# Optimization experiments

Measured on AMD Instinct MI355X. Metric: run time of the kernel, lower is better.

The kernel has to match this reference:

```python
import jax, jax.numpy as jnp
from jax import lax
import numpy as np

NEG_INF = -10000.0
MAX_W = 15          # max_span_width for every marker
M = 5               # num_markers
H = 1024            # encoder hidden size (deberta-v3-large)
B, N = 16, 2048


def _gelu(x):
    return jax.nn.gelu(x, approximate=False)  # torch nn.GELU default (erf)


def _consistency(scores, mask, gamma, width_logits):
    # scores: [B, N] token scores for one marker; mask: [B, N] int
    n = scores.shape[1]
    masked = jnp.where(mask == 0, NEG_INF, scores)
    ww = jax.nn.softmax(width_logits)  # [MAX_W]
    boosts = [masked]
    for w in range(2, min(MAX_W, n) + 1):
        # sliding-window min of width w -> span_mins [B, n-w+1]
        mins = lax.reduce_window(masked, float('inf'), lax.min,
                                 (1, w), (1, 1), 'VALID')
        weighted = mins * ww[w - 2]
        # expand each span-min back to every token it covers via sliding max
        p = jnp.pad(weighted, ((0, 0), (w - 1, w - 1)), constant_values=NEG_INF)
        expanded = lax.reduce_window(p, float('-inf'), lax.max,
                                     (1, w), (1, 1), 'VALID')  # [B, n]
        boosts.append(expanded)
    boost = jnp.max(jnp.stack(boosts, axis=0), axis=0)
    return scores + gamma * boost


def setup_inputs() -> dict:
    key = jax.random.key(0)
    ks = jax.random.split(key, 12)
    s = 0.02
    inp = {
        'h': jax.random.normal(ks[0], (B, N, H), jnp.float32),
        'attention_mask': jnp.ones((B, N), jnp.int32),
        # per-marker token scorers, stacked on leading marker axis
        'W1': jax.random.normal(ks[1], (M, H, 512), jnp.float32) * s,
        'b1': jnp.zeros((M, 512), jnp.float32),
        'W2': jax.random.normal(ks[2], (M, 512, 256), jnp.float32) * s,
        'b2': jnp.zeros((M, 256), jnp.float32),
        'W3': jax.random.normal(ks[3], (M, 256), jnp.float32) * s,
        'b3': jnp.zeros((M,), jnp.float32),
        # span-consistency params
        'gamma': jnp.ones((M,), jnp.float32),
        'width_logits': jax.random.normal(ks[4], (M, MAX_W), jnp.float32) * 0.1,
        # cross-marker attention params
        'corr': jnp.eye(M, dtype=jnp.float32) * 0.5,
        'cw1': jax.random.normal(ks[5], (M, 64), jnp.float32) * 0.1,
        'cb1': jnp.zeros((64,), jnp.float32),
        'cw2': jax.random.normal(ks[6], (64, M), jnp.float32) * 0.1,
        'cb2': jnp.zeros((M,), jnp.float32),
        'gate': jnp.array(0.3, jnp.float32),
    }
    return inp


def reference(h, attention_mask, W1, b1, W2, b2, W3, b3,
              gamma, width_logits, corr, cw1, cb1, cw2, cb2, gate):
    # token scorers (dropout is identity in eval): [M, B, N]
    t1 = _gelu(jnp.einsum('bnh,mhd->mbnd', h, W1) + b1[:, None, None, :])
    t2 = _gelu(jnp.einsum('mbnd,mde->mbne', t1, W2) + b2[:, None, None, :])
    scores = jnp.einsum('mbne,me->mbn', t2, W3) + b3[:, None, None]
    # per-marker span-consistency boost
    boosted = jax.vmap(_consistency, in_axes=(0, None, 0, 0))(
        scores, attention_mask, gamma, width_logits)      # [M, B, N]
    logits = jnp.transpose(boosted, (1, 2, 0))            # [B, N, M]
    # cross-marker attention
    probs = jax.nn.sigmoid(logits)
    correlated = probs @ corr
    refined = _gelu(correlated @ cw1 + cb1) @ cw2 + cb2
    return logits + jax.nn.sigmoid(gate) * refined
```

## Files before the change

kernel.cpp:

```cpp
#include <hip/hip_runtime.h>
#include <math.h>


typedef __bf16 bf16x8 __attribute__((ext_vector_type(8)));
typedef float f32x4 __attribute__((ext_vector_type(4)));

#define NEG_INF_VAL (-10000.0f)

__device__ __forceinline__ unsigned short f2bf(float f) {
  union { float f; unsigned u; } v; v.f = f;
  unsigned r = v.u + 0x7fffu + ((v.u >> 16) & 1u);
  return (unsigned short)(r >> 16);
}
__device__ __forceinline__ float bf2f(unsigned short b) {
  union { unsigned u; float f; } v; v.u = ((unsigned)b) << 16;
  return v.f;
}
__device__ __forceinline__ float gelu_erf(float x) {
  return 0.5f * x * (1.0f + erff(x * 0.7071067811865476f));
}
__device__ __forceinline__ float gelu_fast(float x) {
  float u = 0.7978845608f * x * (1.0f + 0.044715f * x * x);
  float e = __expf(-2.0f * fabsf(u));
  float t = (1.0f - e) / (1.0f + e);
  t = copysignf(t, u);
  return 0.5f * x * (1.0f + t);
}

__global__ __launch_bounds__(256) void k_f32_to_bf16x4(
    const float* __restrict__ in, unsigned short* __restrict__ out, int n4) {
  int i = blockIdx.x * 256 + threadIdx.x;
  if (i >= n4) return;
  float4 v = reinterpret_cast<const float4*>(in)[i];
  ushort4 o;
  o.x = f2bf(v.x); o.y = f2bf(v.y); o.z = f2bf(v.z); o.w = f2bf(v.w);
  reinterpret_cast<ushort4*>(out)[i] = o;
}

__global__ __launch_bounds__(256) void k_transpose_tiled(
    const float* __restrict__ W, unsigned short* __restrict__ Wt,
    int K, int C) {
  __shared__ float tile[32][33];
  const int m = blockIdx.z;
  const int c0 = blockIdx.x * 32, k0 = blockIdx.y * 32;
  const int tx = threadIdx.x & 31, ty = threadIdx.x >> 5;
  const float* Wm = W + (size_t)m * K * C;
#pragma unroll
  for (int r = ty; r < 32; r += 8)
    tile[r][tx] = Wm[(size_t)(k0 + r) * C + c0 + tx];
  __syncthreads();
  unsigned short* Wtm = Wt + (size_t)m * C * K;
#pragma unroll
  for (int r = ty; r < 32; r += 8)
    Wtm[(size_t)(c0 + r) * K + k0 + tx] = f2bf(tile[tx][r]);
}

__device__ __forceinline__ void stage_tile(
    const unsigned short* __restrict__ A, size_t lda,
    const unsigned short* __restrict__ B, size_t ldb,
    int rowA0, int rowB0, int k0,
    unsigned short* As, unsigned short* Bs, int w, int l) {
  const int r = l & 15;
  const int c8 = (l >> 4) * 8;
#pragma unroll
  for (int h = 0; h < 2; ++h) {
    const unsigned short* ga = A + (size_t)(rowA0 + h * 128 + w * 16 + r) * lda + k0 + c8;
    unsigned short* da = As + (h * 8 + w) * 1024 + l * 8;
    __builtin_amdgcn_global_load_lds((const __attribute__((address_space(1))) void*)ga,
                                     (__attribute__((address_space(3))) void*)da, 16, 0, 0);
    __builtin_amdgcn_global_load_lds((const __attribute__((address_space(1))) void*)(ga + 32),
                                     (__attribute__((address_space(3))) void*)(da + 512), 16, 0, 0);
    const unsigned short* gb = B + (size_t)(rowB0 + h * 128 + w * 16 + r) * ldb + k0 + c8;
    unsigned short* db = Bs + (h * 8 + w) * 1024 + l * 8;
    __builtin_amdgcn_global_load_lds((const __attribute__((address_space(1))) void*)gb,
                                     (__attribute__((address_space(3))) void*)db, 16, 0, 0);
    __builtin_amdgcn_global_load_lds((const __attribute__((address_space(1))) void*)(gb + 32),
                                     (__attribute__((address_space(3))) void*)(db + 512), 16, 0, 0);
  }
}

template <bool FUSE_SCORES>
__global__ __launch_bounds__(512) void k_gemm256(
    const unsigned short* __restrict__ A, int lda, int aOffPerM,
    const unsigned short* __restrict__ Bt, int K,
    const float* __restrict__ bias,
    unsigned short* __restrict__ C, int ldc,
    const float* __restrict__ W3, const float* __restrict__ b3,
    float* __restrict__ scoresOut,
    int tilesPerM, int colsPerM, int nColTiles) {
  __shared__ __align__(16) unsigned short As[2][16384];
  __shared__ __align__(16) unsigned short Bs[2][16384];
  __shared__ float sc[256];
  const int t512 = threadIdx.x;
  const int w = t512 >> 6, l = t512 & 63;
  const int wr = w >> 2, wc = w & 3;

  const int nwg = gridDim.x;
  const int cpx = nwg >> 3;
  const int bid = blockIdx.x;
  const int swz = (bid & 7) * cpx + (bid >> 3);
  const int ct = swz % nColTiles, rt = swz / nColTiles;
  const int m = ct / tilesPerM, cb = ct - m * tilesPerM;
  const int gcol0 = m * colsPerM + cb * 256;
  const int row0 = rt * 256;
  const unsigned short* Am = A + (size_t)m * aOffPerM;

  if (FUSE_SCORES && t512 < 256) sc[t512] = 0.f;

  f32x4 acc[8][4] = {};
  const int NT = K >> 6;

  stage_tile(Am, lda, Bt, K, row0, gcol0, 0, As[0], Bs[0], w, l);
  stage_tile(Am, lda, Bt, K, row0, gcol0, 64, As[1], Bs[1], w, l);
  asm volatile("s_waitcnt vmcnt(8)" ::: "memory");
  __builtin_amdgcn_sched_barrier(0);
  __builtin_amdgcn_s_barrier();
  __builtin_amdgcn_sched_barrier(0);

  for (int t = 0; t < NT; ++t) {
    const int p = t & 1;
    bf16x8 af[8][2], bf[4][2];
#pragma unroll
    for (int i = 0; i < 8; ++i)
#pragma unroll
      for (int ks = 0; ks < 2; ++ks)
        af[i][ks] = *reinterpret_cast<const bf16x8*>(&As[p][(wr * 8 + i) * 1024 + ks * 512 + l * 8]);
#pragma unroll
    for (int j = 0; j < 4; ++j)
#pragma unroll
      for (int ks = 0; ks < 2; ++ks)
        bf[j][ks] = *reinterpret_cast<const bf16x8*>(&Bs[p][(wc * 4 + j) * 1024 + ks * 512 + l * 8]);
    asm volatile("s_waitcnt lgkmcnt(0)" ::: "memory");
    __builtin_amdgcn_sched_barrier(0);
    __builtin_amdgcn_s_barrier();
    __builtin_amdgcn_sched_barrier(0);
    if (t + 2 < NT)
      stage_tile(Am, lda, Bt, K, row0, gcol0, (t + 2) * 64, As[p], Bs[p], w, l);
    __builtin_amdgcn_sched_barrier(0);
    __builtin_amdgcn_s_setprio(1);
#pragma unroll
    for (int ks = 0; ks < 2; ++ks)
#pragma unroll
      for (int i = 0; i < 8; ++i)
#pragma unroll
        for (int j = 0; j < 4; ++j)
          acc[i][j] = __builtin_amdgcn_mfma_f32_16x16x32_bf16(af[i][ks], bf[j][ks], acc[i][j], 0, 0, 0);
    __builtin_amdgcn_s_setprio(0);
    __builtin_amdgcn_sched_barrier(0);
    if (t + 1 < NT) {
      if (t + 2 < NT) { asm volatile("s_waitcnt vmcnt(8)" ::: "memory"); }
      else            { asm volatile("s_waitcnt vmcnt(0)" ::: "memory"); }
      __builtin_amdgcn_sched_barrier(0);
      __builtin_amdgcn_s_barrier();
      __builtin_amdgcn_sched_barrier(0);
    }
  }

  if (!FUSE_SCORES) {
    const int orow = (l >> 4) * 4, ocol = l & 15;
#pragma unroll
    for (int i = 0; i < 8; ++i)
#pragma unroll
      for (int j = 0; j < 4; ++j) {
        const int gc = gcol0 + wc * 64 + j * 16 + ocol;
        const float bv = bias[gc];
        const int gr0 = row0 + wr * 128 + i * 16 + orow;
#pragma unroll
        for (int r = 0; r < 4; ++r) {
          float v = gelu_fast(acc[i][j][r] + bv);
          C[(size_t)(gr0 + r) * ldc + gc] = f2bf(v);
        }
      }
  } else {
    const int ocol = l & 15;
#pragma unroll
    for (int i = 0; i < 8; ++i) {
      float rs[4] = {0.f, 0.f, 0.f, 0.f};
#pragma unroll
      for (int j = 0; j < 4; ++j) {
        const int cl = wc * 64 + j * 16 + ocol;
        const float bv = bias[m * 256 + cl];
        const float w3v = W3[m * 256 + cl];
#pragma unroll
        for (int r = 0; r < 4; ++r)
          rs[r] += gelu_fast(acc[i][j][r] + bv) * w3v;
      }
#pragma unroll
      for (int s = 1; s < 16; s <<= 1)
#pragma unroll
        for (int r = 0; r < 4; ++r)
          rs[r] += __shfl_xor(rs[r], s);
      if (ocol == 0) {
        const int lr0 = wr * 128 + i * 16 + (l >> 4) * 4;
#pragma unroll
        for (int r = 0; r < 4; ++r)
          atomicAdd(&sc[lr0 + r], rs[r]);
      }
    }
    __syncthreads();
    if (t512 < 256)
      scoresOut[(size_t)m * 32768 + row0 + t512] = sc[t512] + b3[m];
  }
}

__global__ __launch_bounds__(256) void k_span(
    const float* __restrict__ scores,
    const int* __restrict__ mask,
    const float* __restrict__ gamma,
    const float* __restrict__ wlog,
    float* __restrict__ logits) {
  const int b = blockIdx.x, m = blockIdx.y;
  const int tid = threadIdx.x;
  __shared__ float masked[2048], mins[2048], boost[2048];
  __shared__ float ww[14];
  if (tid == 0) {
    float mx = -1e30f;
    for (int i = 0; i < 15; i++) mx = fmaxf(mx, wlog[m * 15 + i]);
    float e[15], sum = 0.f;
    for (int i = 0; i < 15; i++) { e[i] = expf(wlog[m * 15 + i] - mx); sum += e[i]; }
    for (int i = 0; i < 14; i++) ww[i] = e[i] / sum;
  }
  const float* srow = scores + ((size_t)m * 16 + b) * 2048;
  const int* mrow = mask + (size_t)b * 2048;
  for (int i = tid; i < 2048; i += 256) {
    float s = srow[i];
    float mk = (mrow[i] == 0) ? NEG_INF_VAL : s;
    masked[i] = mk; mins[i] = mk; boost[i] = mk;
  }
  __syncthreads();
  for (int w2 = 2; w2 <= 15; w2++) {
    for (int s = tid; s <= 2048 - w2; s += 256)
      mins[s] = fminf(mins[s], masked[s + w2 - 1]);
    __syncthreads();
    float c = ww[w2 - 2];
    for (int i = tid; i < 2048; i += 256) {
      int lo = i - w2 + 1; if (lo < 0) lo = 0;
      int hi = i; if (hi > 2048 - w2) hi = 2048 - w2;
      float mx = -1e30f;
      for (int s = lo; s <= hi; s++) mx = fmaxf(mx, mins[s]);
      boost[i] = fmaxf(boost[i], mx * c);
    }
    __syncthreads();
  }
  float g = gamma[m];
  for (int i = tid; i < 2048; i += 256)
    logits[((size_t)b * 2048 + i) * 5 + m] = srow[i] + g * boost[i];
}

__global__ __launch_bounds__(256) void k_cross(
    const float* __restrict__ logits, const float* __restrict__ corr,
    const float* __restrict__ cw1, const float* __restrict__ cb1,
    const float* __restrict__ cw2, const float* __restrict__ cb2,
    const float* __restrict__ gate, float* __restrict__ out) {
  __shared__ float s_corr[25], s_cw1[320], s_cb1[64], s_cw2[320], s_cb2[5];
  int tid = threadIdx.x;
  if (tid < 25) s_corr[tid] = corr[tid];
  if (tid < 64) s_cb1[tid] = cb1[tid];
  if (tid < 5)  s_cb2[tid] = cb2[tid];
  for (int i = tid; i < 320; i += 256) { s_cw1[i] = cw1[i]; s_cw2[i] = cw2[i]; }
  __syncthreads();
  int t = blockIdx.x * 256 + tid;
  float lg[5], pr[5];
#pragma unroll
  for (int m = 0; m < 5; m++) {
    lg[m] = logits[(size_t)t * 5 + m];
    pr[m] = 1.f / (1.f + expf(-lg[m]));
  }
  float co[5];
#pragma unroll
  for (int j = 0; j < 5; j++) {
    float s = 0.f;
#pragma unroll
    for (int mm = 0; mm < 5; mm++) s += pr[mm] * s_corr[mm * 5 + j];
    co[j] = s;
  }
  float ref[5];
#pragma unroll
  for (int m = 0; m < 5; m++) ref[m] = s_cb2[m];
  for (int k = 0; k < 64; k++) {
    float h = s_cb1[k];
#pragma unroll
    for (int j = 0; j < 5; j++) h += co[j] * s_cw1[j * 64 + k];
    h = gelu_erf(h);
#pragma unroll
    for (int m = 0; m < 5; m++) ref[m] += h * s_cw2[k * 5 + m];
  }
  float sg = 1.f / (1.f + expf(-gate[0]));
#pragma unroll
  for (int m = 0; m < 5; m++) out[(size_t)t * 5 + m] = lg[m] + sg * ref[m];
}

extern "C" void kernel_launch(void* const* d_in, const int* in_sizes, int n_in,
                              void* d_out, int out_size, void* d_ws, size_t ws_size,
                              hipStream_t stream) {
  const float* h     = (const float*)d_in[0];
  const int*   mask  = (const int*)d_in[1];
  const float* W1    = (const float*)d_in[2];
  const float* b1    = (const float*)d_in[3];
  const float* W2    = (const float*)d_in[4];
  const float* b2    = (const float*)d_in[5];
  const float* W3    = (const float*)d_in[6];
  const float* b3    = (const float*)d_in[7];
  const float* gamma = (const float*)d_in[8];
  const float* wlog  = (const float*)d_in[9];
  const float* corr  = (const float*)d_in[10];
  const float* cw1   = (const float*)d_in[11];
  const float* cb1   = (const float*)d_in[12];
  const float* cw2   = (const float*)d_in[13];
  const float* cb2   = (const float*)d_in[14];
  const float* gate  = (const float*)d_in[15];
  float* out = (float*)d_out;

  char* ws = (char*)d_ws;
  unsigned short* hb  = (unsigned short*)(ws);
  unsigned short* W1t = (unsigned short*)(ws + 67108864);
  unsigned short* W2t = (unsigned short*)(ws + 72351744);
  unsigned short* t1  = (unsigned short*)(ws + 73662464);
  float* scores       = (float*)(ws + 241434624);
  float* logits       = (float*)(ws + 242089984);

  k_f32_to_bf16x4<<<33554432 / 4 / 256, 256, 0, stream>>>(h, hb, 33554432 / 4);
  k_transpose_tiled<<<dim3(16, 32, 5), 256, 0, stream>>>(W1, W1t, 1024, 512);
  k_transpose_tiled<<<dim3(8, 16, 5), 256, 0, stream>>>(W2, W2t, 512, 256);

  k_gemm256<false><<<1280, 512, 0, stream>>>(
      hb, 1024, 0, W1t, 1024, b1, t1, 2560,
      nullptr, nullptr, nullptr, 10, 2560, 10);
  k_gemm256<true><<<640, 512, 0, stream>>>(
      t1, 2560, 512, W2t, 512, b2, nullptr, 0,
      W3, b3, scores, 1, 256, 5);

  k_span<<<dim3(16, 5), 256, 0, stream>>>(scores, mask, gamma, wlog, logits);
  k_cross<<<32768 / 256, 256, 0, stream>>>(logits, corr, cw1, cb1, cw2, cb2, gate, out);
}
```

Baseline: 679.6 us.

## Restructure GEMM mainloop into four sub-phases with interleaved half-tile prefetch

The GEMM main loop is rewritten so each 64-wide K tile is split into four phases (two K halves by two row halves). Each phase loads fewer fragments from LDS, issues part of the next tile's global-to-LDS copies, then runs 16 MFMAs. The trip count becomes a template parameter and the loop is unrolled by two with explicit tail tiles, and pointer increments replace per-stage address recomputation. The goal is to cut register pressure and spread memory traffic across the MFMA stream, at the cost of many more barriers per tile and fragile hand-counted vmcnt values.

```diff
diff --git a/kernel.cpp b/kernel.cpp
--- a/kernel.cpp
+++ b/kernel.cpp
@@ -55,31 +55,112 @@
     Wtm[(size_t)(c0 + r) * K + k0 + tx] = f2bf(tile[tx][r]);
 }
 
-__device__ __forceinline__ void stage_tile(
-    const unsigned short* __restrict__ A, size_t lda,
-    const unsigned short* __restrict__ B, size_t ldb,
-    int rowA0, int rowB0, int k0,
-    unsigned short* As, unsigned short* Bs, int w, int l) {
-  const int r = l & 15;
-  const int c8 = (l >> 4) * 8;
-#pragma unroll
-  for (int h = 0; h < 2; ++h) {
-    const unsigned short* ga = A + (size_t)(rowA0 + h * 128 + w * 16 + r) * lda + k0 + c8;
-    unsigned short* da = As + (h * 8 + w) * 1024 + l * 8;
-    __builtin_amdgcn_global_load_lds((const __attribute__((address_space(1))) void*)ga,
-                                     (__attribute__((address_space(3))) void*)da, 16, 0, 0);
-    __builtin_amdgcn_global_load_lds((const __attribute__((address_space(1))) void*)(ga + 32),
-                                     (__attribute__((address_space(3))) void*)(da + 512), 16, 0, 0);
-    const unsigned short* gb = B + (size_t)(rowB0 + h * 128 + w * 16 + r) * ldb + k0 + c8;
-    unsigned short* db = Bs + (h * 8 + w) * 1024 + l * 8;
-    __builtin_amdgcn_global_load_lds((const __attribute__((address_space(1))) void*)gb,
-                                     (__attribute__((address_space(3))) void*)db, 16, 0, 0);
-    __builtin_amdgcn_global_load_lds((const __attribute__((address_space(1))) void*)(gb + 32),
-                                     (__attribute__((address_space(3))) void*)(db + 512), 16, 0, 0);
-  }
-}
-
-template <bool FUSE_SCORES>
+#define STAGE(GP, LP)                                                        \
+  __builtin_amdgcn_global_load_lds(                                          \
+      (const __attribute__((address_space(1))) void*)(GP),                   \
+      (__attribute__((address_space(3))) void*)(LP), 16, 0, 0)
+
+#define TILE(SLOT, DO_S1, DO_S0, VM1, VM3)                                   \
+  {                                                                          \
+    bf16x8 af[4], bfr[4];                                                    \
+                                               \
+    _Pragma("unroll") for (int j = 0; j < 4; ++j)                            \
+      bfr[j] = *reinterpret_cast<const bf16x8*>(                             \
+          &Bs[SLOT][(wc * 4 + j) * 1024 + l8]);                              \
+    _Pragma("unroll") for (int i = 0; i < 4; ++i)                            \
+      af[i] = *reinterpret_cast<const bf16x8*>(                              \
+          &As[SLOT][(wr * 8 + i) * 1024 + l8]);                              \
+    if (DO_S1) {                                                             \
+      STAGE(pA0 + 96, &As[1 - (SLOT)][(0 * 8 + w) * 1024 + 512 + l8]);       \
+      STAGE(pA1 + 96, &As[1 - (SLOT)][(1 * 8 + w) * 1024 + 512 + l8]);       \
+    }                                                                        \
+    __builtin_amdgcn_s_barrier();                                            \
+    __builtin_amdgcn_sched_barrier(0);                                       \
+    asm volatile("s_waitcnt lgkmcnt(0)" ::: "memory");                       \
+    __builtin_amdgcn_sched_barrier(0);                                       \
+    __builtin_amdgcn_s_setprio(1);                                           \
+    _Pragma("unroll") for (int i = 0; i < 4; ++i)                            \
+      _Pragma("unroll") for (int j = 0; j < 4; ++j)                          \
+        acc[i][j] = __builtin_amdgcn_mfma_f32_16x16x32_bf16(                 \
+            af[i], bfr[j], acc[i][j], 0, 0, 0);                              \
+    __builtin_amdgcn_s_setprio(0);                                           \
+    __builtin_amdgcn_sched_barrier(0);                                       \
+    __builtin_amdgcn_s_barrier();                                            \
+    __builtin_amdgcn_sched_barrier(0);                                       \
+                                               \
+    _Pragma("unroll") for (int i = 0; i < 4; ++i)                            \
+      af[i] = *reinterpret_cast<const bf16x8*>(                              \
+          &As[SLOT][(wr * 8 + 4 + i) * 1024 + l8]);                          \
+    if (DO_S1) {                                                             \
+      STAGE(pB0 + 96, &Bs[1 - (SLOT)][(0 * 8 + w) * 1024 + 512 + l8]);       \
+      STAGE(pB1 + 96, &Bs[1 - (SLOT)][(1 * 8 + w) * 1024 + 512 + l8]);       \
+    }                                                                        \
+    __builtin_amdgcn_s_barrier();                                            \
+    __builtin_amdgcn_sched_barrier(0);                                       \
+    asm volatile("s_waitcnt lgkmcnt(0)" ::: "memory");                       \
+    __builtin_amdgcn_sched_barrier(0);                                       \
+    __builtin_amdgcn_s_setprio(1);                                           \
+    _Pragma("unroll") for (int i = 0; i < 4; ++i)                            \
+      _Pragma("unroll") for (int j = 0; j < 4; ++j)                          \
+        acc[4 + i][j] = __builtin_amdgcn_mfma_f32_16x16x32_bf16(             \
+            af[i], bfr[j], acc[4 + i][j], 0, 0, 0);                          \
+    __builtin_amdgcn_s_setprio(0);                                           \
+    __builtin_amdgcn_sched_barrier(0);                                       \
+    asm volatile("s_waitcnt vmcnt(" VM1 ")" ::: "memory");                   \
+    __builtin_amdgcn_sched_barrier(0);                                       \
+    __builtin_amdgcn_s_barrier();                                            \
+    __builtin_amdgcn_sched_barrier(0);                                       \
+                                               \
+    _Pragma("unroll") for (int j = 0; j < 4; ++j)                            \
+      bfr[j] = *reinterpret_cast<const bf16x8*>(                             \
+          &Bs[SLOT][(wc * 4 + j) * 1024 + 512 + l8]);                        \
+    _Pragma("unroll") for (int i = 0; i < 4; ++i)                            \
+      af[i] = *reinterpret_cast<const bf16x8*>(                              \
+          &As[SLOT][(wr * 8 + i) * 1024 + 512 + l8]);                        \
+    if (DO_S0) {                                                             \
+      STAGE(pA0 + 128, &As[SLOT][(0 * 8 + w) * 1024 + l8]);                  \
+      STAGE(pA1 + 128, &As[SLOT][(1 * 8 + w) * 1024 + l8]);                  \
+    }                                                                        \
+    __builtin_amdgcn_s_barrier();                                            \
+    __builtin_amdgcn_sched_barrier(0);                                       \
+    asm volatile("s_waitcnt lgkmcnt(0)" ::: "memory");                       \
+    __builtin_amdgcn_sched_barrier(0);                                       \
+    __builtin_amdgcn_s_setprio(1);                                           \
+    _Pragma("unroll") for (int i = 0; i < 4; ++i)                            \
+      _Pragma("unroll") for (int j = 0; j < 4; ++j)                          \
+        acc[i][j] = __builtin_amdgcn_mfma_f32_16x16x32_bf16(                 \
+            af[i], bfr[j], acc[i][j], 0, 0, 0);                              \
+    __builtin_amdgcn_s_setprio(0);                                           \
+    __builtin_amdgcn_sched_barrier(0);                                       \
+    __builtin_amdgcn_s_barrier();                                            \
+    __builtin_amdgcn_sched_barrier(0);                                       \
+                                               \
+    _Pragma("unroll") for (int i = 0; i < 4; ++i)                            \
+      af[i] = *reinterpret_cast<const bf16x8*>(                              \
+          &As[SLOT][(wr * 8 + 4 + i) * 1024 + 512 + l8]);                    \
+    if (DO_S0) {                                                             \
+      STAGE(pB0 + 128, &Bs[SLOT][(0 * 8 + w) * 1024 + l8]);                  \
+      STAGE(pB1 + 128, &Bs[SLOT][(1 * 8 + w) * 1024 + l8]);                  \
+    }                                                                        \
+    __builtin_amdgcn_s_barrier();                                            \
+    __builtin_amdgcn_sched_barrier(0);                                       \
+    asm volatile("s_waitcnt lgkmcnt(0)" ::: "memory");                       \
+    __builtin_amdgcn_sched_barrier(0);                                       \
+    __builtin_amdgcn_s_setprio(1);                                           \
+    _Pragma("unroll") for (int i = 0; i < 4; ++i)                            \
+      _Pragma("unroll") for (int j = 0; j < 4; ++j)                          \
+        acc[4 + i][j] = __builtin_amdgcn_mfma_f32_16x16x32_bf16(             \
+            af[i], bfr[j], acc[4 + i][j], 0, 0, 0);                          \
+    __builtin_amdgcn_s_setprio(0);                                           \
+    __builtin_amdgcn_sched_barrier(0);                                       \
+    asm volatile("s_waitcnt vmcnt(" VM3 ")" ::: "memory");                   \
+    __builtin_amdgcn_sched_barrier(0);                                       \
+    __builtin_amdgcn_s_barrier();                                            \
+    __builtin_amdgcn_sched_barrier(0);                                       \
+    pA0 += 64; pA1 += 64; pB0 += 64; pB1 += 64;                              \
+  }
+
+template <bool FUSE_SCORES, int NT>
 __global__ __launch_bounds__(512) void k_gemm256(
     const unsigned short* __restrict__ A, int lda, int aOffPerM,
     const unsigned short* __restrict__ Bt, int K,
@@ -94,6 +175,7 @@
   const int t512 = threadIdx.x;
   const int w = t512 >> 6, l = t512 & 63;
   const int wr = w >> 2, wc = w & 3;
+  const int l8 = l * 8;
 
   const int nwg = gridDim.x;
   const int cpx = nwg >> 3;
@@ -108,53 +190,38 @@
   if (FUSE_SCORES && t512 < 256) sc[t512] = 0.f;
 
   f32x4 acc[8][4] = {};
-  const int NT = K >> 6;
-
-  stage_tile(Am, lda, Bt, K, row0, gcol0, 0, As[0], Bs[0], w, l);
-  stage_tile(Am, lda, Bt, K, row0, gcol0, 64, As[1], Bs[1], w, l);
+
+  const int r = l & 15;
+  const int c8 = (l >> 4) * 8;
+  const unsigned short* pA0 = Am + (size_t)(row0 + w * 16 + r) * lda + c8;
+  const unsigned short* pA1 = Am + (size_t)(row0 + 128 + w * 16 + r) * lda + c8;
+  const unsigned short* pB0 = Bt + (size_t)(gcol0 + w * 16 + r) * (size_t)K + c8;
+  const unsigned short* pB1 = Bt + (size_t)(gcol0 + 128 + w * 16 + r) * (size_t)K + c8;
+
+  STAGE(pA0,      &As[0][(0 * 8 + w) * 1024 + l8]);
+  STAGE(pA1,      &As[0][(1 * 8 + w) * 1024 + l8]);
+  STAGE(pB0,      &Bs[0][(0 * 8 + w) * 1024 + l8]);
+  STAGE(pB1,      &Bs[0][(1 * 8 + w) * 1024 + l8]);
+  STAGE(pA0 + 32, &As[0][(0 * 8 + w) * 1024 + 512 + l8]);
+  STAGE(pA1 + 32, &As[0][(1 * 8 + w) * 1024 + 512 + l8]);
+  STAGE(pB0 + 32, &Bs[0][(0 * 8 + w) * 1024 + 512 + l8]);
+  STAGE(pB1 + 32, &Bs[0][(1 * 8 + w) * 1024 + 512 + l8]);
+  STAGE(pA0 + 64, &As[1][(0 * 8 + w) * 1024 + l8]);
+  STAGE(pA1 + 64, &As[1][(1 * 8 + w) * 1024 + l8]);
+  STAGE(pB0 + 64, &Bs[1][(0 * 8 + w) * 1024 + l8]);
+  STAGE(pB1 + 64, &Bs[1][(1 * 8 + w) * 1024 + l8]);
   asm volatile("s_waitcnt vmcnt(8)" ::: "memory");
   __builtin_amdgcn_sched_barrier(0);
   __builtin_amdgcn_s_barrier();
   __builtin_amdgcn_sched_barrier(0);
 
-  for (int t = 0; t < NT; ++t) {
-    const int p = t & 1;
-    bf16x8 af[8][2], bf[4][2];
-#pragma unroll
-    for (int i = 0; i < 8; ++i)
-#pragma unroll
-      for (int ks = 0; ks < 2; ++ks)
-        af[i][ks] = *reinterpret_cast<const bf16x8*>(&As[p][(wr * 8 + i) * 1024 + ks * 512 + l * 8]);
-#pragma unroll
-    for (int j = 0; j < 4; ++j)
-#pragma unroll
-      for (int ks = 0; ks < 2; ++ks)
-        bf[j][ks] = *reinterpret_cast<const bf16x8*>(&Bs[p][(wc * 4 + j) * 1024 + ks * 512 + l * 8]);
-    asm volatile("s_waitcnt lgkmcnt(0)" ::: "memory");
-    __builtin_amdgcn_sched_barrier(0);
-    __builtin_amdgcn_s_barrier();
-    __builtin_amdgcn_sched_barrier(0);
-    if (t + 2 < NT)
-      stage_tile(Am, lda, Bt, K, row0, gcol0, (t + 2) * 64, As[p], Bs[p], w, l);
-    __builtin_amdgcn_sched_barrier(0);
-    __builtin_amdgcn_s_setprio(1);
-#pragma unroll
-    for (int ks = 0; ks < 2; ++ks)
-#pragma unroll
-      for (int i = 0; i < 8; ++i)
-#pragma unroll
-        for (int j = 0; j < 4; ++j)
-          acc[i][j] = __builtin_amdgcn_mfma_f32_16x16x32_bf16(af[i][ks], bf[j][ks], acc[i][j], 0, 0, 0);
-    __builtin_amdgcn_s_setprio(0);
-    __builtin_amdgcn_sched_barrier(0);
-    if (t + 1 < NT) {
-      if (t + 2 < NT) { asm volatile("s_waitcnt vmcnt(8)" ::: "memory"); }
-      else            { asm volatile("s_waitcnt vmcnt(0)" ::: "memory"); }
-      __builtin_amdgcn_sched_barrier(0);
-      __builtin_amdgcn_s_barrier();
-      __builtin_amdgcn_sched_barrier(0);
-    }
-  }
+#pragma unroll 1
+  for (int t = 0; t < NT - 2; t += 2) {
+    TILE(0, 1, 1, "8", "8");
+    TILE(1, 1, 1, "8", "8");
+  }
+  TILE(0, 1, 0, "8", "4");
+  TILE(1, 0, 0, "0", "0");
 
   if (!FUSE_SCORES) {
     const int orow = (l >> 4) * 4, ocol = l & 15;
@@ -166,9 +233,9 @@
         const float bv = bias[gc];
         const int gr0 = row0 + wr * 128 + i * 16 + orow;
 #pragma unroll
-        for (int r = 0; r < 4; ++r) {
-          float v = gelu_fast(acc[i][j][r] + bv);
-          C[(size_t)(gr0 + r) * ldc + gc] = f2bf(v);
+        for (int rr = 0; rr < 4; ++rr) {
+          float v = gelu_fast(acc[i][j][rr] + bv);
+          C[(size_t)(gr0 + rr) * ldc + gc] = f2bf(v);
         }
       }
   } else {
@@ -182,19 +249,19 @@
         const float bv = bias[m * 256 + cl];
         const float w3v = W3[m * 256 + cl];
 #pragma unroll
-        for (int r = 0; r < 4; ++r)
-          rs[r] += gelu_fast(acc[i][j][r] + bv) * w3v;
+        for (int rr = 0; rr < 4; ++rr)
+          rs[rr] += gelu_fast(acc[i][j][rr] + bv) * w3v;
       }
 #pragma unroll
       for (int s = 1; s < 16; s <<= 1)
 #pragma unroll
-        for (int r = 0; r < 4; ++r)
-          rs[r] += __shfl_xor(rs[r], s);
+        for (int rr = 0; rr < 4; ++rr)
+          rs[rr] += __shfl_xor(rs[rr], s);
       if (ocol == 0) {
         const int lr0 = wr * 128 + i * 16 + (l >> 4) * 4;
 #pragma unroll
-        for (int r = 0; r < 4; ++r)
-          atomicAdd(&sc[lr0 + r], rs[r]);
+        for (int rr = 0; rr < 4; ++rr)
+          atomicAdd(&sc[lr0 + rr], rs[rr]);
       }
     }
     __syncthreads();
@@ -323,10 +390,10 @@
   k_transpose_tiled<<<dim3(16, 32, 5), 256, 0, stream>>>(W1, W1t, 1024, 512);
   k_transpose_tiled<<<dim3(8, 16, 5), 256, 0, stream>>>(W2, W2t, 512, 256);
 
-  k_gemm256<false><<<1280, 512, 0, stream>>>(
+  k_gemm256<false, 16><<<1280, 512, 0, stream>>>(
       hb, 1024, 0, W1t, 1024, b1, t1, 2560,
       nullptr, nullptr, nullptr, 10, 2560, 10);
-  k_gemm256<true><<<640, 512, 0, stream>>>(
+  k_gemm256<true, 8><<<640, 512, 0, stream>>>(
       t1, 2560, 512, W2t, 512, b2, nullptr, 0,
       W3, b3, scores, 1, 256, 5);
 
```

After: 681.5 us. About the same (+0.3%).
